# Kernel tuning notes

Hardware: AMD Instinct MI355X
Metric: run time of the kernel (lower is better)

Reference implementation:

```python
import jax, jax.numpy as jnp
import numpy as np

T, B = 128, 256          # frames, batch (free dims)
C_IN = 201               # in_features
KD = 3                   # keypoint_dimensionality
NK = C_IN // KD          # 67 keypoints = attention seq len
E = 8                    # d_pose_embed
H = 2                    # heads
DH = E // H              # head dim = 4
L = 12                   # encoder layers
FF = 2 * E               # 16
OUT = 128                # output_size
EPS = 1e-5


def setup_inputs() -> dict:
    key = jax.random.key(0)
    ks = jax.random.split(key, 12)
    s = 0.1
    return {
        "pose_clip": jax.random.normal(ks[0], (T, B, C_IN), jnp.float32),
        "embed_w": jax.random.normal(ks[1], (E, KD), jnp.float32) * s,
        "embed_b": jax.random.normal(ks[2], (E,), jnp.float32) * s,
        "in_proj_w": jax.random.normal(ks[3], (L, 3 * E, E), jnp.float32) * s,
        "in_proj_b": jax.random.normal(ks[4], (L, 3 * E), jnp.float32) * s,
        "attn_out_w": jax.random.normal(ks[5], (L, E, E), jnp.float32) * s,
        "attn_out_b": jax.random.normal(ks[6], (L, E), jnp.float32) * s,
        "ff1_w": jax.random.normal(ks[7], (L, FF, E), jnp.float32) * s,
        "ff1_b": jax.random.normal(ks[8], (L, FF), jnp.float32) * s,
        "ff2_w": jax.random.normal(ks[9], (L, E, FF), jnp.float32) * s,
        "ff2_b": jax.random.normal(ks[10], (L, E), jnp.float32) * s,
        "ln1_g": jnp.ones((L, E), jnp.float32),
        "ln1_b": jnp.zeros((L, E), jnp.float32),
        "ln2_g": jnp.ones((L, E), jnp.float32),
        "ln2_b": jnp.zeros((L, E), jnp.float32),
        "out_w": jax.random.normal(ks[11], (OUT, NK * E), jnp.float32) * s,
        "out_b": jnp.zeros((OUT,), jnp.float32),
    }


def _ln(x, g, b):
    m = jnp.mean(x, axis=-1, keepdims=True)
    v = jnp.mean(jnp.square(x - m), axis=-1, keepdims=True)
    return (x - m) * jax.lax.rsqrt(v + EPS) * g + b


def _encoder(x, layer_params):
    # x: [S, N, E]; post-LN TransformerEncoderLayer, relu activation, no dropout (eval)
    def step(h, p):
        ipw, ipb, aow, aob, f1w, f1b, f2w, f2b, g1, b1, g2, b2 = p
        S, N, _ = h.shape
        qkv = h @ ipw.T + ipb                      # [S, N, 3E]
        q, k, v = jnp.split(qkv, 3, axis=-1)
        q = q.reshape(S, N, H, DH)
        k = k.reshape(S, N, H, DH)
        v = v.reshape(S, N, H, DH)
        scores = jnp.einsum('snhd,tnhd->nhst', q, k) / np.sqrt(DH).astype(h.dtype)
        attn = jax.nn.softmax(scores, axis=-1)
        o = jnp.einsum('nhst,tnhd->snhd', attn, v).reshape(S, N, E)
        o = o @ aow.T + aob
        h = _ln(h + o, g1, b1)
        ff = jax.nn.relu(h @ f1w.T + f1b) @ f2w.T + f2b
        h = _ln(h + ff, g2, b2)
        return h, None
    x, _ = jax.lax.scan(step, x, layer_params)
    return x


def reference(pose_clip, embed_w, embed_b, in_proj_w, in_proj_b, attn_out_w,
              attn_out_b, ff1_w, ff1_b, ff2_w, ff2_b, ln1_g, ln1_b, ln2_g,
              ln2_b, out_w, out_b):
    t, b, c = pose_clip.shape
    nk = c // KD
    # [t,b,c] -> [t*b, nk, 3] -> [nk, t*b, 3]  (seq=keypoints, batch=t*b)
    x = pose_clip.reshape(t * b, nk, KD).transpose(1, 0, 2)
    x = x @ embed_w.T + embed_b                    # [nk, t*b, E]
    layer_params = (in_proj_w, in_proj_b, attn_out_w, attn_out_b,
                    ff1_w, ff1_b, ff2_w, ff2_b, ln1_g, ln1_b, ln2_g, ln2_b)
    x = _encoder(x, layer_params)
    x = x.transpose(1, 0, 2).reshape(t, b, nk * E)  # [t, b, 536]
    return jnp.tanh(x @ out_w.T + out_b)            # [t, b, 128]
```

## Files before the change

### kernel.cpp

```cpp
#include <hip/hip_runtime.h>
#include <math.h>

#define NTOT 32768
#define CIN  201
#define S    67
#define E    8
#define H    2
#define L    12
#define FF   16
#define OUTC 128
#define KF   536
#define EPB  7
#define THREADS 512
#define NPAIR 33

typedef float v2f __attribute__((ext_vector_type(2)));

#if __has_builtin(__builtin_amdgcn_exp2f)
#define EXP2F(x) __builtin_amdgcn_exp2f(x)
#else
#define EXP2F(x) exp2f(x)
#endif
#if __has_builtin(__builtin_amdgcn_rcpf)
#define RCPF(x) __builtin_amdgcn_rcpf(x)
#else
#define RCPF(x) (1.0f/(x))
#endif
#if __has_builtin(__builtin_amdgcn_rsqf)
#define RSQF(x) __builtin_amdgcn_rsqf(x)
#else
#define RSQF(x) rsqrtf(x)
#endif

#define QSCALE 0.7213475204444817f

__device__ __forceinline__ void layernorm8(float* xr, const float* __restrict__ gg,
                                           const float* __restrict__ bb) {
    float m = 0.f;
    #pragma unroll
    for (int e = 0; e < E; ++e) m += xr[e];
    m *= 0.125f;
    float v = 0.f;
    #pragma unroll
    for (int e = 0; e < E; ++e) { float d = xr[e] - m; v += d * d; }
    v *= 0.125f;
    float rs = RSQF(v + 1e-5f);
    #pragma unroll
    for (int e = 0; e < E; ++e) xr[e] = (xr[e] - m) * rs * gg[e] + bb[e];
}

__global__ void prep_kernel(const float* __restrict__ ipw, const float* __restrict__ aow,
                            const float* __restrict__ f1w, const float* __restrict__ f2w,
                            float* __restrict__ wp)
{
    int idx = blockIdx.x * 256 + threadIdx.x;
    if (idx >= L * 512) return;
    int l = idx >> 9, r = idx & 511;
    float v;
    if (r < 192)      { int e = r / 24, j = r % 24;          v = ipw[l*192 + j*8 + e]; }
    else if (r < 256) { int q = r - 192; int e2 = q / 8, e = q % 8; v = aow[l*64 + e*8 + e2]; }
    else if (r < 384) { int q = r - 256; int e = q / 16, f = q % 16; v = f1w[l*128 + f*8 + e]; }
    else              { int q = r - 384; int f = q / 8,  e = q % 8;  v = f2w[l*128 + e*16 + f]; }
    wp[idx] = v;
}

__global__ __launch_bounds__(THREADS, 4)
void enc_kernel(const float* __restrict__ pose,
                const float* __restrict__ ew,  const float* __restrict__ ebias,
                const float* __restrict__ wp,  const float* __restrict__ ipb,
                const float* __restrict__ aob,
                const float* __restrict__ f1b, const float* __restrict__ f2b,
                const float* __restrict__ g1,  const float* __restrict__ b1,
                const float* __restrict__ g2,  const float* __restrict__ b2,
                float* __restrict__ xf)
{
    __shared__ float4 buf[4][EPB * H][NPAIR + 1];

    const int lid = threadIdx.x;
    const int g   = lid / S;
    const int s   = lid - g * S;
    const int n   = blockIdx.x * EPB + g;
    const bool active = (g < EPB) && (n < NTOT);
    const int ii = s >> 1, hf = s & 1;

    float xr[E];
    if (active) {
        const float* p = pose + (size_t)n * CIN + 3 * s;
        float r0 = p[0], r1 = p[1], r2 = p[2];
        #pragma unroll
        for (int e = 0; e < E; ++e)
            xr[e] = ebias[e] + r0 * ew[e*3+0] + r1 * ew[e*3+1] + r2 * ew[e*3+2];
    }

    #pragma unroll 1
    for (int l = 0; l < L; ++l) {
        const float* WL   = wp + l * 512;
        const float* qkvt = WL;
        const float* aowt = WL + 192;
        const float* f1t  = WL + 256;
        const float* f2t  = WL + 384;
        const float* bq   = ipb + l * 24;

        float qsc[E];
        if (active) {
            v2f xs[E];
            #pragma unroll
            for (int e = 0; e < E; ++e) xs[e] = (v2f){xr[e], xr[e]};

            v2f qkv[12];
            #pragma unroll
            for (int p = 0; p < 12; ++p) {
                v2f a = *(const v2f*)(bq + 2*p);
                #pragma unroll
                for (int e = 0; e < E; ++e)
                    a += xs[e] * (*(const v2f*)(qkvt + e*24 + 2*p));
                qkv[p] = a;
            }
            #pragma unroll
            for (int p = 0; p < 4; ++p) {
                qsc[2*p]   = qkv[p].x * QSCALE;
                qsc[2*p+1] = qkv[p].y * QSCALE;
            }
            #pragma unroll
            for (int h = 0; h < H; ++h) {
                const int gh = g*2 + h;
                float* pKA = (float*)&buf[0][gh][ii];
                float* pKB = (float*)&buf[1][gh][ii];
                float* pVA = (float*)&buf[2][gh][ii];
                float* pVB = (float*)&buf[3][gh][ii];
                pKA[hf] = qkv[4+2*h].x;  pKA[2+hf] = qkv[4+2*h].y;
                pKB[hf] = qkv[5+2*h].x;  pKB[2+hf] = qkv[5+2*h].y;
                pVA[hf] = qkv[8+2*h].x;  pVA[2+hf] = qkv[8+2*h].y;
                pVB[hf] = qkv[9+2*h].x;  pVB[2+hf] = qkv[9+2*h].y;
            }
        }
        __syncthreads();

        if (active) {
            float oo[E];
            #pragma unroll
            for (int h = 0; h < H; ++h) {
                const int gh = g*2 + h;
                const float4* KA = buf[0][gh];
                const float4* KB = buf[1][gh];
                const float4* VA = buf[2][gh];
                const float4* VB = buf[3][gh];
                const float q0s = qsc[4*h+0], q1s = qsc[4*h+1];
                const float q2s = qsc[4*h+2], q3s = qsc[4*h+3];
                const v2f qx2 = {q0s, q0s}, qy2 = {q1s, q1s};
                const v2f qz2 = {q2s, q2s}, qw2 = {q3s, q3s};
                v2f l2 = {0.f, 0.f};
                v2f ox = {0.f,0.f}, oy = {0.f,0.f}, oz = {0.f,0.f}, ow = {0.f,0.f};
                #pragma unroll
                for (int i = 0; i < NPAIR; ++i) {
                    float4 ka = KA[i], kb = KB[i];
                    float4 va = VA[i], vb = VB[i];
                    v2f sc = qx2 * *(const v2f*)&ka.x + qy2 * *(const v2f*)&ka.z
                           + qz2 * *(const v2f*)&kb.x + qw2 * *(const v2f*)&kb.z;
                    v2f e2;
                    e2.x = EXP2F(sc.x);
                    e2.y = EXP2F(sc.y);
                    l2 += e2;
                    ox += e2 * *(const v2f*)&va.x;
                    oy += e2 * *(const v2f*)&va.z;
                    oz += e2 * *(const v2f*)&vb.x;
                    ow += e2 * *(const v2f*)&vb.z;
                }
                float4 ka = KA[NPAIR], kb = KB[NPAIR];
                float4 va = VA[NPAIR], vb = VB[NPAIR];
                float sc1 = q0s*ka.x + q1s*ka.z + q2s*kb.x + q3s*kb.z;
                float e1  = EXP2F(sc1);
                float lsum = l2.x + l2.y + e1;
                float inv  = RCPF(lsum);
                oo[4*h+0] = (ox.x + ox.y + e1*va.x) * inv;
                oo[4*h+1] = (oy.x + oy.y + e1*va.z) * inv;
                oo[4*h+2] = (oz.x + oz.y + e1*vb.x) * inv;
                oo[4*h+3] = (ow.x + ow.y + e1*vb.z) * inv;
            }

            {
                const float* ba = aob + l*E;
                v2f os[E];
                #pragma unroll
                for (int e2 = 0; e2 < E; ++e2) os[e2] = (v2f){oo[e2], oo[e2]};
                #pragma unroll
                for (int p = 0; p < 4; ++p) {
                    v2f a = *(const v2f*)(ba + 2*p);
                    #pragma unroll
                    for (int e2 = 0; e2 < E; ++e2)
                        a += os[e2] * (*(const v2f*)(aowt + e2*8 + 2*p));
                    xr[2*p]   += a.x;
                    xr[2*p+1] += a.y;
                }
            }
            layernorm8(xr, g1 + l*E, b1 + l*E);

            {
                const float* fb1 = f1b + l*FF;
                const float* fb2 = f2b + l*E;
                v2f xs[E];
                #pragma unroll
                for (int e = 0; e < E; ++e) xs[e] = (v2f){xr[e], xr[e]};
                v2f t1p[8];
                #pragma unroll
                for (int p = 0; p < 8; ++p) {
                    v2f a = *(const v2f*)(fb1 + 2*p);
                    #pragma unroll
                    for (int e = 0; e < E; ++e)
                        a += xs[e] * (*(const v2f*)(f1t + e*16 + 2*p));
                    a.x = fmaxf(a.x, 0.f);
                    a.y = fmaxf(a.y, 0.f);
                    t1p[p] = a;
                }
                v2f ts[FF];
                #pragma unroll
                for (int p = 0; p < 8; ++p) {
                    ts[2*p]   = (v2f){t1p[p].x, t1p[p].x};
                    ts[2*p+1] = (v2f){t1p[p].y, t1p[p].y};
                }
                #pragma unroll
                for (int p = 0; p < 4; ++p) {
                    v2f a = *(const v2f*)(fb2 + 2*p);
                    #pragma unroll
                    for (int f = 0; f < FF; ++f)
                        a += ts[f] * (*(const v2f*)(f2t + f*8 + 2*p));
                    xr[2*p]   += a.x;
                    xr[2*p+1] += a.y;
                }
            }
            layernorm8(xr, g2 + l*E, b2 + l*E);
        }
        __syncthreads();
    }

    if (active) {
        float4* o4 = (float4*)(xf + (size_t)n * KF + s * E);
        o4[0] = make_float4(xr[0], xr[1], xr[2], xr[3]);
        o4[1] = make_float4(xr[4], xr[5], xr[6], xr[7]);
    }
}

__global__ void tr_kernel(const float* __restrict__ ow, float* __restrict__ wt)
{
    int i = blockIdx.x * 256 + threadIdx.x;
    if (i < OUTC * KF) {
        int c = i / KF, k = i - c * KF;
        wt[k * OUTC + c] = ow[i];
    }
}

__global__ __launch_bounds__(256, 4)
void out_kernel(const float* __restrict__ xf, const float* __restrict__ wt,
                const float* __restrict__ ob, float* __restrict__ out)
{
    __shared__ float Xs[32][68];
    const int lid = threadIdx.x;
    const int tx  = lid & 31;
    const int ty  = lid >> 5;
    const int n0  = blockIdx.x * 32;

    float acc[4][4] = {};

    #pragma unroll 1
    for (int kc = 0; kc < 9; ++kc) {
        const int kb = kc * 64;
        const int kw = (kc < 8) ? 64 : 24;
        __syncthreads();
        const int nvec = 32 * (kw >> 2);
        for (int i = lid; i < nvec; i += 256) {
            int r = i / (kw >> 2), kq = i - r * (kw >> 2);
            *(float4*)&Xs[r][kq*4] =
                *(const float4*)&xf[(size_t)(n0 + r) * KF + kb + kq*4];
        }
        __syncthreads();
        #pragma unroll 4
        for (int k = 0; k < kw; ++k) {
            float4 w4 = *(const float4*)&wt[(size_t)(kb + k) * OUTC + tx*4];
            #pragma unroll
            for (int i = 0; i < 4; ++i) {
                float x = Xs[ty*4 + i][k];
                acc[i][0] += x*w4.x; acc[i][1] += x*w4.y;
                acc[i][2] += x*w4.z; acc[i][3] += x*w4.w;
            }
        }
    }

    const float4 bb = *(const float4*)&ob[tx*4];
    #pragma unroll
    for (int i = 0; i < 4; ++i) {
        int r = n0 + ty*4 + i;
        float4 v;
        v.x = tanhf(acc[i][0] + bb.x);
        v.y = tanhf(acc[i][1] + bb.y);
        v.z = tanhf(acc[i][2] + bb.z);
        v.w = tanhf(acc[i][3] + bb.w);
        *(float4*)(out + (size_t)r * OUTC + tx*4) = v;
    }
}

extern "C" void kernel_launch(void* const* d_in, const int* in_sizes, int n_in,
                              void* d_out, int out_size, void* d_ws, size_t ws_size,
                              hipStream_t stream) {
    (void)in_sizes; (void)n_in; (void)out_size; (void)ws_size;
    const float* pose = (const float*)d_in[0];
    const float* ew   = (const float*)d_in[1];
    const float* eb   = (const float*)d_in[2];
    const float* ipw  = (const float*)d_in[3];
    const float* ipb  = (const float*)d_in[4];
    const float* aow  = (const float*)d_in[5];
    const float* aob  = (const float*)d_in[6];
    const float* f1w  = (const float*)d_in[7];
    const float* f1b  = (const float*)d_in[8];
    const float* f2w  = (const float*)d_in[9];
    const float* f2b  = (const float*)d_in[10];
    const float* g1   = (const float*)d_in[11];
    const float* b1   = (const float*)d_in[12];
    const float* g2   = (const float*)d_in[13];
    const float* b2   = (const float*)d_in[14];
    const float* ow   = (const float*)d_in[15];
    const float* ob   = (const float*)d_in[16];

    float* xf = (float*)d_ws;
    float* wt = xf + (size_t)NTOT * KF;
    float* wp = wt + (size_t)KF * OUTC;

    prep_kernel<<<(L*512 + 255)/256, 256, 0, stream>>>(ipw, aow, f1w, f2w, wp);
    const int grid1 = (NTOT + EPB - 1) / EPB;
    enc_kernel<<<grid1, THREADS, 0, stream>>>(pose, ew, eb, wp, ipb, aob,
                                              f1b, f2b, g1, b1, g2, b2, xf);
    tr_kernel<<<(OUTC*KF + 255)/256, 256, 0, stream>>>(ow, wt);
    out_kernel<<<NTOT / 32, 256, 0, stream>>>(xf, wt, ob, (float*)d_out);
}
```

Measured before the change: 1.447 ms.

## Compute encoder attention with fp16 MFMA, one wavefront per sequence

The encoder kernel is restructured so that each 64-lane wavefront owns one sequence, with each lane handling one or two keypoint rows. The QK^T and PV products now run on 16x16x16 fp16 MFMA instructions, with Q/K/V stored as fp16 in shared memory and padded to 80 positions. The block-wide __syncthreads is removed in favour of wave-local data flow. The padded keys give exp(0)=1 per padded column, which is corrected by subtracting 13 from the softmax sum. The trade-offs are reduced precision in attention and redundant MFMA work on padding; the second row per lane is computed for every lane even though only 3 lanes use it.

```diff
diff --git a/kernel.cpp b/kernel.cpp
--- a/kernel.cpp
+++ b/kernel.cpp
@@ -10,11 +10,16 @@
 #define FF   16
 #define OUTC 128
 #define KF   536
-#define EPB  7
-#define THREADS 512
-#define NPAIR 33
-
-typedef float v2f __attribute__((ext_vector_type(2)));
+#define WPB  4
+#define THREADS 256
+#define SP   80
+#define NT   5
+
+typedef float    v2f __attribute__((ext_vector_type(2)));
+typedef float    v4f __attribute__((ext_vector_type(4)));
+typedef _Float16 v2h __attribute__((ext_vector_type(2)));
+typedef _Float16 v4h __attribute__((ext_vector_type(4)));
+typedef __fp16   v2hf __attribute__((ext_vector_type(2)));
 
 #if __has_builtin(__builtin_amdgcn_exp2f)
 #define EXP2F(x) __builtin_amdgcn_exp2f(x)
@@ -32,10 +37,34 @@
 #define RSQF(x) rsqrtf(x)
 #endif
 
+static __device__ __forceinline__ v4f MFMA16(v4h a, v4h b, v4f c) {
+#if defined(__HIP_DEVICE_COMPILE__)
+    return __builtin_amdgcn_mfma_f32_16x16x16f16(a, b, c, 0, 0, 0);
+#else
+    (void)a; (void)b;
+    return c;
+#endif
+}
+
 #define QSCALE 0.7213475204444817f
 
-__device__ __forceinline__ void layernorm8(float* xr, const float* __restrict__ gg,
-                                           const float* __restrict__ bb) {
+static __device__ __forceinline__ v2h CVTPK(float a, float b) {
+#if __has_builtin(__builtin_amdgcn_cvt_pkrtz)
+    union { v2hf f; v2h h; } x;
+    x.f = __builtin_amdgcn_cvt_pkrtz(a, b);
+    return x.h;
+#else
+    return (v2h){(_Float16)a, (_Float16)b};
+#endif
+}
+
+__device__ __forceinline__ v2f sp(float x) { return (v2f){x, x}; }
+__device__ __forceinline__ unsigned int h2u(v2h h){ union{v2h h;unsigned int u;}x; x.h=h; return x.u; }
+__device__ __forceinline__ v4h ld4h(const uint2* p){ union{uint2 u;v4h h;}x; x.u=*p; return x.h; }
+__device__ __forceinline__ v4h zero4h(){ return (v4h){(_Float16)0.f,(_Float16)0.f,(_Float16)0.f,(_Float16)0.f}; }
+
+__device__ __forceinline__ void ln8(float* xr, const float* __restrict__ gg,
+                                    const float* __restrict__ bb) {
     float m = 0.f;
     #pragma unroll
     for (int e = 0; e < E; ++e) m += xr[e];
@@ -64,6 +93,73 @@
     wp[idx] = v;
 }
 
+__device__ __forceinline__ void stage1_row(
+    const float* __restrict__ qkvt, const float* __restrict__ bq,
+    const float* xr, int r, bool pred,
+    uint2 (*Qw)[SP], uint2 (*Kw)[SP], _Float16 (*Vw)[SP])
+{
+    v2f qkv[12];
+    #pragma unroll
+    for (int p = 0; p < 12; ++p) {
+        v2f a = *(const v2f*)(bq + 2*p);
+        #pragma unroll
+        for (int e = 0; e < E; ++e) a += sp(xr[e]) * (*(const v2f*)(qkvt + e*24 + 2*p));
+        qkv[p] = a;
+    }
+    if (pred) {
+        #pragma unroll
+        for (int h = 0; h < H; ++h) {
+            uint2 qw, kw;
+            qw.x = h2u(CVTPK(qkv[2*h].x * QSCALE, qkv[2*h].y * QSCALE));
+            qw.y = h2u(CVTPK(qkv[2*h+1].x * QSCALE, qkv[2*h+1].y * QSCALE));
+            kw.x = h2u(CVTPK(qkv[4+2*h].x, qkv[4+2*h].y));
+            kw.y = h2u(CVTPK(qkv[5+2*h].x, qkv[5+2*h].y));
+            Qw[h][r] = qw;
+            Kw[h][r] = kw;
+            Vw[h*4+0][r] = (_Float16)qkv[8+2*h].x;
+            Vw[h*4+1][r] = (_Float16)qkv[8+2*h].y;
+            Vw[h*4+2][r] = (_Float16)qkv[9+2*h].x;
+            Vw[h*4+3][r] = (_Float16)qkv[9+2*h].y;
+        }
+    }
+}
+
+__device__ __forceinline__ void stage3_row(
+    const float* __restrict__ WL, const float* __restrict__ ba,
+    const float* __restrict__ fb1, const float* __restrict__ fb2,
+    const float* __restrict__ g1l, const float* __restrict__ b1l,
+    const float* __restrict__ g2l, const float* __restrict__ b2l,
+    const float* o8, float* xr)
+{
+    const float* aowt = WL + 192;
+    const float* f1t  = WL + 256;
+    const float* f2t  = WL + 384;
+    #pragma unroll
+    for (int p = 0; p < 4; ++p) {
+        v2f a = *(const v2f*)(ba + 2*p);
+        #pragma unroll
+        for (int e2 = 0; e2 < E; ++e2) a += sp(o8[e2]) * (*(const v2f*)(aowt + e2*8 + 2*p));
+        xr[2*p] += a.x; xr[2*p+1] += a.y;
+    }
+    ln8(xr, g1l, b1l);
+    float t1[FF];
+    #pragma unroll
+    for (int p = 0; p < 8; ++p) {
+        v2f a = *(const v2f*)(fb1 + 2*p);
+        #pragma unroll
+        for (int e = 0; e < E; ++e) a += sp(xr[e]) * (*(const v2f*)(f1t + e*16 + 2*p));
+        t1[2*p] = fmaxf(a.x, 0.f); t1[2*p+1] = fmaxf(a.y, 0.f);
+    }
+    #pragma unroll
+    for (int p = 0; p < 4; ++p) {
+        v2f a = *(const v2f*)(fb2 + 2*p);
+        #pragma unroll
+        for (int f = 0; f < FF; ++f) a += sp(t1[f]) * (*(const v2f*)(f2t + f*8 + 2*p));
+        xr[2*p] += a.x; xr[2*p+1] += a.y;
+    }
+    ln8(xr, g2l, b2l);
+}
+
 __global__ __launch_bounds__(THREADS, 4)
 void enc_kernel(const float* __restrict__ pose,
                 const float* __restrict__ ew,  const float* __restrict__ ebias,
@@ -74,169 +170,113 @@
                 const float* __restrict__ g2,  const float* __restrict__ b2,
                 float* __restrict__ xf)
 {
-    __shared__ float4 buf[4][EPB * H][NPAIR + 1];
-
-    const int lid = threadIdx.x;
-    const int g   = lid / S;
-    const int s   = lid - g * S;
-    const int n   = blockIdx.x * EPB + g;
-    const bool active = (g < EPB) && (n < NTOT);
-    const int ii = s >> 1, hf = s & 1;
-
-    float xr[E];
-    if (active) {
-        const float* p = pose + (size_t)n * CIN + 3 * s;
-        float r0 = p[0], r1 = p[1], r2 = p[2];
+    __shared__ uint2 Qs[WPB][H][SP];
+    __shared__ uint2 Ks[WPB][H][SP];
+    __shared__ __align__(16) _Float16 Vs[WPB][H*4][SP];
+    __shared__ float4 Os[WPB][H][SP];
+
+    const int lane = threadIdx.x & 63;
+    const int w    = threadIdx.x >> 6;
+    const int n    = blockIdx.x * WPB + w;
+    const int tq   = lane & 15, quad = lane >> 4;
+    const int r1c  = (lane < 3) ? (64 + lane) : 66;
+    const bool tact = (lane < 3);
+
+    if (lane < 13) {
+        int t = S + lane;
+        #pragma unroll
+        for (int h = 0; h < H; ++h) {
+            Qs[w][h][t] = make_uint2(0u, 0u);
+            Ks[w][h][t] = make_uint2(0u, 0u);
+        }
+        #pragma unroll
+        for (int d = 0; d < 8; ++d) Vs[w][d][t] = (_Float16)0.f;
+    }
+
+    float xr0[E], xr1[E];
+    {
+        const float* p = pose + (size_t)n * CIN + 3 * lane;
         #pragma unroll
         for (int e = 0; e < E; ++e)
-            xr[e] = ebias[e] + r0 * ew[e*3+0] + r1 * ew[e*3+1] + r2 * ew[e*3+2];
+            xr0[e] = ebias[e] + p[0]*ew[e*3+0] + p[1]*ew[e*3+1] + p[2]*ew[e*3+2];
+        const float* p1 = pose + (size_t)n * CIN + 3 * r1c;
+        #pragma unroll
+        for (int e = 0; e < E; ++e)
+            xr1[e] = ebias[e] + p1[0]*ew[e*3+0] + p1[1]*ew[e*3+1] + p1[2]*ew[e*3+2];
     }
 
     #pragma unroll 1
     for (int l = 0; l < L; ++l) {
-        const float* WL   = wp + l * 512;
-        const float* qkvt = WL;
-        const float* aowt = WL + 192;
-        const float* f1t  = WL + 256;
-        const float* f2t  = WL + 384;
-        const float* bq   = ipb + l * 24;
-
-        float qsc[E];
-        if (active) {
-            v2f xs[E];
+        const float* WL = wp + l * 512;
+        const float* bq = ipb + l * 24;
+
+        stage1_row(WL, bq, xr0, lane, true, Qs[w], Ks[w], Vs[w]);
+        stage1_row(WL, bq, xr1, r1c, tact, Qs[w], Ks[w], Vs[w]);
+
+        #pragma unroll 1
+        for (int h = 0; h < H; ++h) {
+            v4h Ka[NT], Va[NT];
             #pragma unroll
-            for (int e = 0; e < E; ++e) xs[e] = (v2f){xr[e], xr[e]};
-
-            v2f qkv[12];
-            #pragma unroll
-            for (int p = 0; p < 12; ++p) {
-                v2f a = *(const v2f*)(bq + 2*p);
+            for (int t = 0; t < NT; ++t) {
+                Ka[t] = zero4h();
+                if (quad == 0) Ka[t] = ld4h(&Ks[w][h][t*16 + tq]);
+                Va[t] = zero4h();
+                if (tq < 4) Va[t] = *(const v4h*)&Vs[w][h*4 + tq][t*16 + quad*4];
+            }
+            #pragma unroll 1
+            for (int sg = 0; sg < NT; ++sg) {
+                v4h bqf = zero4h();
+                if (quad == 0) bqf = ld4h(&Qs[w][h][sg*16 + tq]);
+                v4f acc = {0.f, 0.f, 0.f, 0.f};
+                const v4f zf = {0.f, 0.f, 0.f, 0.f};
+                float lsum = 0.f;
                 #pragma unroll
-                for (int e = 0; e < E; ++e)
-                    a += xs[e] * (*(const v2f*)(qkvt + e*24 + 2*p));
-                qkv[p] = a;
+                for (int t = 0; t < NT; ++t) {
+                    v4f c = MFMA16(Ka[t], bqf, zf);
+                    float e0 = EXP2F(c.x), e1 = EXP2F(c.y);
+                    float e2 = EXP2F(c.z), e3 = EXP2F(c.w);
+                    lsum += (e0 + e1) + (e2 + e3);
+                    union { v2h h2[2]; v4h h4; } pu;
+                    pu.h2[0] = CVTPK(e0, e1);
+                    pu.h2[1] = CVTPK(e2, e3);
+                    acc = MFMA16(Va[t], pu.h4, acc);
+                }
+                lsum += __shfl_xor(lsum, 16, 64);
+                lsum += __shfl_xor(lsum, 32, 64);
+                float inv = RCPF(lsum - 13.0f);
+                if (quad == 0)
+                    Os[w][h][sg*16 + tq] =
+                        make_float4(acc.x*inv, acc.y*inv, acc.z*inv, acc.w*inv);
             }
-            #pragma unroll
-            for (int p = 0; p < 4; ++p) {
-                qsc[2*p]   = qkv[p].x * QSCALE;
-                qsc[2*p+1] = qkv[p].y * QSCALE;
-            }
-            #pragma unroll
-            for (int h = 0; h < H; ++h) {
-                const int gh = g*2 + h;
-                float* pKA = (float*)&buf[0][gh][ii];
-                float* pKB = (float*)&buf[1][gh][ii];
-                float* pVA = (float*)&buf[2][gh][ii];
-                float* pVB = (float*)&buf[3][gh][ii];
-                pKA[hf] = qkv[4+2*h].x;  pKA[2+hf] = qkv[4+2*h].y;
-                pKB[hf] = qkv[5+2*h].x;  pKB[2+hf] = qkv[5+2*h].y;
-                pVA[hf] = qkv[8+2*h].x;  pVA[2+hf] = qkv[8+2*h].y;
-                pVB[hf] = qkv[9+2*h].x;  pVB[2+hf] = qkv[9+2*h].y;
-            }
-        }
-        __syncthreads();
-
-        if (active) {
-            float oo[E];
-            #pragma unroll
-            for (int h = 0; h < H; ++h) {
-                const int gh = g*2 + h;
-                const float4* KA = buf[0][gh];
-                const float4* KB = buf[1][gh];
-                const float4* VA = buf[2][gh];
-                const float4* VB = buf[3][gh];
-                const float q0s = qsc[4*h+0], q1s = qsc[4*h+1];
-                const float q2s = qsc[4*h+2], q3s = qsc[4*h+3];
-                const v2f qx2 = {q0s, q0s}, qy2 = {q1s, q1s};
-                const v2f qz2 = {q2s, q2s}, qw2 = {q3s, q3s};
-                v2f l2 = {0.f, 0.f};
-                v2f ox = {0.f,0.f}, oy = {0.f,0.f}, oz = {0.f,0.f}, ow = {0.f,0.f};
-                #pragma unroll
-                for (int i = 0; i < NPAIR; ++i) {
-                    float4 ka = KA[i], kb = KB[i];
-                    float4 va = VA[i], vb = VB[i];
-                    v2f sc = qx2 * *(const v2f*)&ka.x + qy2 * *(const v2f*)&ka.z
-                           + qz2 * *(const v2f*)&kb.x + qw2 * *(const v2f*)&kb.z;
-                    v2f e2;
-                    e2.x = EXP2F(sc.x);
-                    e2.y = EXP2F(sc.y);
-                    l2 += e2;
-                    ox += e2 * *(const v2f*)&va.x;
-                    oy += e2 * *(const v2f*)&va.z;
-                    oz += e2 * *(const v2f*)&vb.x;
-                    ow += e2 * *(const v2f*)&vb.z;
-                }
-                float4 ka = KA[NPAIR], kb = KB[NPAIR];
-                float4 va = VA[NPAIR], vb = VB[NPAIR];
-                float sc1 = q0s*ka.x + q1s*ka.z + q2s*kb.x + q3s*kb.z;
-                float e1  = EXP2F(sc1);
-                float lsum = l2.x + l2.y + e1;
-                float inv  = RCPF(lsum);
-                oo[4*h+0] = (ox.x + ox.y + e1*va.x) * inv;
-                oo[4*h+1] = (oy.x + oy.y + e1*va.z) * inv;
-                oo[4*h+2] = (oz.x + oz.y + e1*vb.x) * inv;
-                oo[4*h+3] = (ow.x + ow.y + e1*vb.z) * inv;
-            }
-
-            {
-                const float* ba = aob + l*E;
-                v2f os[E];
-                #pragma unroll
-                for (int e2 = 0; e2 < E; ++e2) os[e2] = (v2f){oo[e2], oo[e2]};
-                #pragma unroll
-                for (int p = 0; p < 4; ++p) {
-                    v2f a = *(const v2f*)(ba + 2*p);
-                    #pragma unroll
-                    for (int e2 = 0; e2 < E; ++e2)
-                        a += os[e2] * (*(const v2f*)(aowt + e2*8 + 2*p));
-                    xr[2*p]   += a.x;
-                    xr[2*p+1] += a.y;
-                }
-            }
-            layernorm8(xr, g1 + l*E, b1 + l*E);
-
-            {
-                const float* fb1 = f1b + l*FF;
-                const float* fb2 = f2b + l*E;
-                v2f xs[E];
-                #pragma unroll
-                for (int e = 0; e < E; ++e) xs[e] = (v2f){xr[e], xr[e]};
-                v2f t1p[8];
-                #pragma unroll
-                for (int p = 0; p < 8; ++p) {
-                    v2f a = *(const v2f*)(fb1 + 2*p);
-                    #pragma unroll
-                    for (int e = 0; e < E; ++e)
-                        a += xs[e] * (*(const v2f*)(f1t + e*16 + 2*p));
-                    a.x = fmaxf(a.x, 0.f);
-                    a.y = fmaxf(a.y, 0.f);
-                    t1p[p] = a;
-                }
-                v2f ts[FF];
-                #pragma unroll
-                for (int p = 0; p < 8; ++p) {
-                    ts[2*p]   = (v2f){t1p[p].x, t1p[p].x};
-                    ts[2*p+1] = (v2f){t1p[p].y, t1p[p].y};
-                }
-                #pragma unroll
-                for (int p = 0; p < 4; ++p) {
-                    v2f a = *(const v2f*)(fb2 + 2*p);
-                    #pragma unroll
-                    for (int f = 0; f < FF; ++f)
-                        a += ts[f] * (*(const v2f*)(f2t + f*8 + 2*p));
-                    xr[2*p]   += a.x;
-                    xr[2*p+1] += a.y;
-                }
-            }
-            layernorm8(xr, g2 + l*E, b2 + l*E);
-        }
-        __syncthreads();
-    }
-
-    if (active) {
-        float4* o4 = (float4*)(xf + (size_t)n * KF + s * E);
-        o4[0] = make_float4(xr[0], xr[1], xr[2], xr[3]);
-        o4[1] = make_float4(xr[4], xr[5], xr[6], xr[7]);
+        }
+
+        {
+            float o8[E];
+            float4 a = Os[w][0][lane];
+            float4 b = Os[w][1][lane];
+            o8[0]=a.x; o8[1]=a.y; o8[2]=a.z; o8[3]=a.w;
+            o8[4]=b.x; o8[5]=b.y; o8[6]=b.z; o8[7]=b.w;
+            stage3_row(WL, aob+l*8, f1b+l*16, f2b+l*8,
+                       g1+l*8, b1+l*8, g2+l*8, b2+l*8, o8, xr0);
+            float o8b[E];
+            float4 a2 = Os[w][0][r1c];
+            float4 b2v = Os[w][1][r1c];
+            o8b[0]=a2.x; o8b[1]=a2.y; o8b[2]=a2.z; o8b[3]=a2.w;
+            o8b[4]=b2v.x; o8b[5]=b2v.y; o8b[6]=b2v.z; o8b[7]=b2v.w;
+            stage3_row(WL, aob+l*8, f1b+l*16, f2b+l*8,
+                       g1+l*8, b1+l*8, g2+l*8, b2+l*8, o8b, xr1);
+        }
+    }
+
+    {
+        float* dst = xf + (size_t)n * KF + lane * E;
+        *(float4*)(dst + 0) = make_float4(xr0[0], xr0[1], xr0[2], xr0[3]);
+        *(float4*)(dst + 4) = make_float4(xr0[4], xr0[5], xr0[6], xr0[7]);
+        if (tact) {
+            float* dst2 = xf + (size_t)n * KF + (64 + lane) * E;
+            *(float4*)(dst2 + 0) = make_float4(xr1[0], xr1[1], xr1[2], xr1[3]);
+            *(float4*)(dst2 + 4) = make_float4(xr1[4], xr1[5], xr1[6], xr1[7]);
+        }
     }
 }
 
@@ -325,9 +365,8 @@
     float* wp = wt + (size_t)KF * OUTC;
 
     prep_kernel<<<(L*512 + 255)/256, 256, 0, stream>>>(ipw, aow, f1w, f2w, wp);
-    const int grid1 = (NTOT + EPB - 1) / EPB;
-    enc_kernel<<<grid1, THREADS, 0, stream>>>(pose, ew, eb, wp, ipb, aob,
-                                              f1b, f2b, g1, b1, g2, b2, xf);
+    enc_kernel<<<NTOT / WPB, THREADS, 0, stream>>>(pose, ew, eb, wp, ipb, aob,
+                                                   f1b, f2b, g1, b1, g2, b2, xf);
     tr_kernel<<<(OUTC*KF + 255)/256, 256, 0, stream>>>(ow, wt);
     out_kernel<<<NTOT / 32, 256, 0, stream>>>(xf, wt, ob, (float*)d_out);
 }
```

New measurement: 2.135 ms. 1.48x slower.
